# Kernel tuning notes

Hardware: AMD Instinct MI355X
Metric: run time of the kernel (lower is better)

Reference implementation:

```python
import jax, jax.numpy as jnp
import numpy as np

B, T, D = 256, 128, 64
H, A, O = 512, 128, 32


def setup_inputs() -> dict:
    key = jax.random.key(0)
    ks = jax.random.split(key, 16)
    u = lambda k, sh, lo, hi: jax.random.uniform(k, sh, jnp.float32, lo, hi)
    return {
        "x_states": jax.random.normal(ks[0], (B, T, D), jnp.float32),
        "x_dts": jax.random.uniform(ks[1], (B, T), jnp.float32) * 0.1,
        # StepwiseAttention params (stored [in, out])
        "Wq": u(ks[2], (D, A), -0.1, 0.1), "bq": u(ks[3], (A,), -0.1, 0.1),
        "Wk": u(ks[4], (H, A), -0.1, 0.1), "bk": u(ks[5], (A,), -0.1, 0.1),
        "Wv": u(ks[6], (H, A), -0.1, 0.1), "bv": u(ks[7], (A,), -0.1, 0.1),
        # LTCAttentionCell params
        "W_gd": u(ks[8], (D + H + A, 2 * H), -0.1, 0.1),
        "b_gd": u(ks[9], (2 * H,), -0.1, 0.1),
        "W_tau": u(ks[10], (H, H), -0.1, 0.1),
        "b_tau": u(ks[11], (H,), -0.1, 0.1),
        "gleak": u(ks[12], (H,), 0.001, 1.0),
        "cm": u(ks[13], (H,), 0.4, 0.6),
        # output head
        "W_fc": u(ks[14], (H, O), -0.1, 0.1),
        "b_fc": u(ks[15], (O,), -0.1, 0.1),
    }


def _forward(x_states, x_dts, Wq, bq, Wk, bk, Wv, bv,
             W_gd, b_gd, W_tau, b_tau, gleak, cm, W_fc, b_fc):
    scale = jnp.sqrt(jnp.asarray(A, jnp.float32))
    leak = jax.nn.softplus(cm) + jax.nn.softplus(gleak)  # [H]

    def dhdt(h, x_t, ctx):
        combined = jnp.concatenate([x_t, h, ctx], axis=1)        # [B, D+H+A]
        gd = combined @ W_gd + b_gd                              # [B, 2H]
        gate, dyn = jnp.split(gd, 2, axis=1)
        tau = jax.nn.softplus(h @ W_tau + b_tau)                 # [B, H]
        num = jax.nn.sigmoid(gate) * jnp.tanh(dyn) - h
        return num / (tau + leak + 1e-6)

    def step(carry, inp):
        h, hist = carry            # h [B,H], hist [B,T,H]
        t, x_t, dt = inp           # t scalar, x_t [B,D], dt [B]
        # stepwise attention over history h_1..h_t
        Q = x_t @ Wq + bq                                        # [B, A]
        K = hist @ Wk + bk                                       # [B, T, A]
        V = hist @ Wv + bv                                       # [B, T, A]
        scores = jnp.einsum('ba,bta->bt', Q, K) / scale          # [B, T]
        valid = jnp.arange(T) < t
        scores = jnp.where(valid[None, :], scores, -1e9)
        w = jax.nn.softmax(scores, axis=-1)
        ctx = jnp.einsum('bt,bta->ba', w, V)
        ctx = jnp.where(t > 0, ctx, jnp.zeros_like(ctx))         # empty history -> 0
        # one RK4 step (torchdiffeq 'rk4' = 3/8-rule variant), step size dt per sample
        dtc = dt[:, None]
        k1 = dhdt(h, x_t, ctx)
        k2 = dhdt(h + dtc * k1 / 3.0, x_t, ctx)
        k3 = dhdt(h + dtc * (k2 - k1 / 3.0), x_t, ctx)
        k4 = dhdt(h + dtc * (k1 - k2 + k3), x_t, ctx)
        h_next = h + dtc * (k1 + 3.0 * k2 + 3.0 * k3 + k4) / 8.0
        hist = jax.lax.dynamic_update_slice(hist, h_next[:, None, :], (0, t, 0))
        return (h_next, hist), None

    h0 = jnp.zeros((B, H), jnp.float32)
    hist0 = jnp.zeros((B, T, H), jnp.float32)
    xs = (jnp.arange(T), jnp.swapaxes(x_states, 0, 1), jnp.swapaxes(x_dts, 0, 1))
    (h_final, _), _ = jax.lax.scan(step, (h0, hist0), xs)
    return h_final @ W_fc + b_fc                                 # [B, O]


def reference(x_states, x_dts, Wq, bq, Wk, bk, Wv, bv,
              W_gd, b_gd, W_tau, b_tau, gleak, cm, W_fc, b_fc):
    return _forward(x_states, x_dts, Wq, bq, Wk, bk, Wv, bv,
                    W_gd, b_gd, W_tau, b_tau, gleak, cm, W_fc, b_fc)
```

## Files before the change

kernel.cpp:

```cpp
#include <hip/hip_runtime.h>
#include <math.h>

#define B_ 256
#define T_ 128
#define D_ 64
#define H_ 512
#define A_ 128
#define O_ 32

typedef __attribute__((ext_vector_type(8))) short short8;
typedef __attribute__((ext_vector_type(8))) unsigned short ushort8;
typedef __attribute__((ext_vector_type(4))) float floatx4;
typedef __attribute__((ext_vector_type(4))) unsigned int uintx4;
typedef unsigned long long ull;

__device__ __forceinline__ float sp_(float x) {
    return fmaxf(x, 0.f) + log1pf(expf(-fabsf(x)));
}
__device__ __forceinline__ float sigm_(float x) {
    return 1.f / (1.f + expf(-x));
}
__device__ __forceinline__ unsigned short f2bf_(float f) {
    unsigned int u = __float_as_uint(f);
    return (unsigned short)((u + 0x7FFFu + ((u >> 16) & 1u)) >> 16);
}
__device__ __forceinline__ float bf2f_(unsigned short u) {
    return __uint_as_float(((unsigned)u) << 16);
}

__device__ __forceinline__ void ld16sc(uintx4& d, const void* p) {
    asm volatile("global_load_dwordx4 %0, %1, off sc0 sc1"
                 : "=v"(d) : "v"(p) : "memory");
}
__device__ __forceinline__ void ld4sc(float& d, const void* p) {
    asm volatile("global_load_dword %0, %1, off sc0 sc1"
                 : "=v"(d) : "v"(p) : "memory");
}
__device__ __forceinline__ void vmwait4(uintx4& a, uintx4& b, uintx4& c,
                                        uintx4& d) {
    asm volatile("s_waitcnt vmcnt(0)"
                 : "+v"(a), "+v"(b), "+v"(c), "+v"(d)::"memory");
}
__device__ __forceinline__ void vmwait8(uintx4& a, uintx4& b, uintx4& c,
                                        uintx4& d, uintx4& e, uintx4& f,
                                        uintx4& g, uintx4& h) {
    asm volatile("s_waitcnt vmcnt(0)"
                 : "+v"(a), "+v"(b), "+v"(c), "+v"(d), "+v"(e), "+v"(f),
                   "+v"(g), "+v"(h)::"memory");
}
__device__ __forceinline__ void vmwait16f(float& a0, float& a1, float& a2,
                                          float& a3, float& a4, float& a5,
                                          float& a6, float& a7, float& b0,
                                          float& b1, float& b2, float& b3,
                                          float& b4, float& b5, float& b6,
                                          float& b7) {
    asm volatile("s_waitcnt vmcnt(0)"
                 : "+v"(a0), "+v"(a1), "+v"(a2), "+v"(a3), "+v"(a4), "+v"(a5),
                   "+v"(a6), "+v"(a7), "+v"(b0), "+v"(b1), "+v"(b2), "+v"(b3),
                   "+v"(b4), "+v"(b5), "+v"(b6), "+v"(b7)::"memory");
}
__device__ __forceinline__ floatx4 u2f_(uintx4 u) {
    union { uintx4 u; floatx4 f; } c;
    c.u = u;
    return c.f;
}

__device__ __forceinline__ void stf_(float* p, float v) {
    __hip_atomic_store(p, v, __ATOMIC_RELAXED, __HIP_MEMORY_SCOPE_SYSTEM);
}
__device__ __forceinline__ void st64_(ull* p, ull v) {
    __hip_atomic_store(p, v, __ATOMIC_RELAXED, __HIP_MEMORY_SCOPE_SYSTEM);
}

__global__ void init_kernel(unsigned short* __restrict__ hpack,
                            unsigned* __restrict__ bar) {
    int i = blockIdx.x * 256 + threadIdx.x;
    if (i < B_ * H_) hpack[i] = 0;
    if (i < 8192) bar[i] = 0u;
}

__global__ void pack_w_kernel(const float* __restrict__ W_gd,
                              const float* __restrict__ W_tau,
                              const float* __restrict__ Wk,
                              const float* __restrict__ Wv,
                              unsigned short* __restrict__ Wpack) {
    int gid = blockIdx.x * 256 + threadIdx.x;
    if (gid >= 1114112) return;
    int j = gid & 7;
    int l = (gid >> 3) & 63;
    int kpart = (l >> 4) * 8 + j;
    int npart = l & 15;
    float v;
    if (gid < 786432) {
        int f = gid >> 9;
        int s = f % 3;
        int rem = f / 3;
        int kb = rem & 15, ct = rem >> 4;
        int k = kb * 32 + kpart;
        int c = ct * 16 + npart;
        if (s == 0)      v = W_gd[(size_t)(D_ + k) * 1024 + c];
        else if (s == 1) v = W_gd[(size_t)(D_ + k) * 1024 + 512 + c];
        else             v = W_tau[(size_t)k * 512 + c];
    } else if (gid < 851968) {
        int r = gid - 786432;
        int f = r >> 9;
        int s = f & 1, kb = (f >> 1) & 1, ct = f >> 2;
        int k = kb * 32 + kpart;
        int c = ct * 16 + npart;
        v = W_gd[(size_t)k * 1024 + s * 512 + c];
    } else if (gid < 983040) {
        int r = gid - 851968;
        int f = r >> 9;
        int s = f & 1, kb = (f >> 1) & 3, ct = f >> 3;
        int k = kb * 32 + kpart;
        int c = ct * 16 + npart;
        v = W_gd[(size_t)(D_ + H_ + k) * 1024 + s * 512 + c];
    } else {
        int r = gid - 983040;
        int f = r >> 9;
        int kb = f & 15, c4 = f >> 4;
        int k = kb * 32 + kpart;
        int n = (c4 & 7) * 16 + npart;
        v = (c4 < 8) ? Wk[(size_t)k * A_ + n] : Wv[(size_t)k * A_ + n];
    }
    Wpack[gid] = f2bf_(v);
}

__device__ __forceinline__ void gsyncF(unsigned* flags, int j, unsigned cnt) {
    asm volatile("s_waitcnt vmcnt(0)" ::: "memory");
    __syncthreads();
    if (threadIdx.x == 0)
        __hip_atomic_store(flags + j * 64, cnt, __ATOMIC_RELAXED,
                           __HIP_MEMORY_SCOPE_SYSTEM);
    if (threadIdx.x < 8) {
        while (__hip_atomic_load(flags + threadIdx.x * 64, __ATOMIC_RELAXED,
                                 __HIP_MEMORY_SCOPE_SYSTEM) < cnt) {
            __builtin_amdgcn_s_sleep(1);
        }
    }
    __syncthreads();
}

struct P {
    const float *x, *dts, *Wq, *bq, *bk, *bv, *b_gd, *b_tau, *gleak, *cm,
        *W_fc, *b_fc;
    float *h, *ctx, *out, *Kpart, *Vpart;
    unsigned short* Kh;
    const unsigned short *Wy, *Wx, *Wc, *Wkv;
    unsigned short *hpack, *yapack, *ybpack;
    unsigned* bar;
};

__global__ __launch_bounds__(256, 1) void fused_kernel(P p) {
    const int tid = threadIdx.x;
    const int bid = blockIdx.x;
    const int lane = tid & 63;
    const int wave = tid >> 6;
    const int g = bid & 15;
    const int j = bid >> 4;
    const int ct = j * 4 + wave;
    unsigned* flags = p.bar + g * 512;
    unsigned cnt = 0;

    __shared__ float WqL[D_ * 129];
    __shared__ float xs4[2][D_];
    __shared__ float q4[2][A_];
    __shared__ float sc4[2][T_];
    __shared__ float red[2][2];
    __shared__ __align__(16) unsigned short AsL[32 * 256];
    __shared__ __align__(16) unsigned short ypbuf[4 * 256];
    __shared__ __align__(16) unsigned short As2[2 * 512];
    __shared__ unsigned short VhL[2][A_][136];

    const int quad = lane >> 4;
    const int c = ct * 16 + (lane & 15);
    const float btau = p.b_tau[c];
    const float lk = sp_(p.cm[c]) + sp_(p.gleak[c]) + 1e-6f;
    const float bgd_g = p.b_gd[c];
    const float bgd_d = p.b_gd[512 + c];
    const int aoff = (quad >> 1) * 256 + (lane & 15) * 16 + (quad & 1) * 8;
    const int ypw = wave * 256 + (lane & 15);

    const int sub = tid >> 7;
    const int tl = tid & 127;
    const int r = g * 16 + j * 2 + sub;
    const int rrow = r & 15;

    short8 wg[16], wd[16], wt[16];
    short8 wxg[2], wxd[2], wcg[4], wcd[4];
    {
        const short8* Wy8 = (const short8*)p.Wy;
        #pragma unroll
        for (int kb = 0; kb < 16; ++kb) {
            wg[kb] = Wy8[((ct * 16 + kb) * 3 + 0) * 64 + lane];
            wd[kb] = Wy8[((ct * 16 + kb) * 3 + 1) * 64 + lane];
            wt[kb] = Wy8[((ct * 16 + kb) * 3 + 2) * 64 + lane];
        }
        const short8* Wx8 = (const short8*)p.Wx;
        const short8* Wc8 = (const short8*)p.Wc;
        #pragma unroll
        for (int kb = 0; kb < 2; ++kb) {
            wxg[kb] = Wx8[((ct * 2 + kb) * 2 + 0) * 64 + lane];
            wxd[kb] = Wx8[((ct * 2 + kb) * 2 + 1) * 64 + lane];
        }
        #pragma unroll
        for (int kb = 0; kb < 4; ++kb) {
            wcg[kb] = Wc8[((ct * 4 + kb) * 2 + 0) * 64 + lane];
            wcd[kb] = Wc8[((ct * 4 + kb) * 2 + 1) * 64 + lane];
        }
    }

    for (int i = tid; i < D_ * A_; i += 256) {
        int d = i >> 7, a = i & 127;
        WqL[d * 129 + a] = p.Wq[i];
    }

    floatx4 hreg = {0.f, 0.f, 0.f, 0.f};
    floatx4 rk1, rk2, rk3, baseg, based, ycur, dt4;

    const short8* Wkv8 = (const short8*)p.Wkv;

    __syncthreads();

    for (int t = 0; t < T_; ++t) {
        {
            if (t > 0) {
                float kk[8], vv[8];
                #pragma unroll
                for (int jj = 0; jj < 8; ++jj) {
                    ld4sc(kk[jj],
                          p.Kpart + ((g * 8 + jj) * 16 + rrow) * 128 + tl);
                    ld4sc(vv[jj],
                          p.Vpart + ((g * 8 + jj) * 16 + rrow) * 128 + tl);
                }
                vmwait16f(kk[0], kk[1], kk[2], kk[3], kk[4], kk[5], kk[6],
                          kk[7], vv[0], vv[1], vv[2], vv[3], vv[4], vv[5],
                          vv[6], vv[7]);
                float ks = p.bk[tl], vs = p.bv[tl];
                #pragma unroll
                for (int jj = 0; jj < 8; ++jj) {
                    ks += kk[jj];
                    vs += vv[jj];
                }
                p.Kh[(size_t)(r * T_ + (t - 1)) * A_ + tl] = f2bf_(ks);
                VhL[sub][tl][t - 1] = f2bf_(vs);
            }
            if (tl < 16)
                ((float4*)xs4[sub])[tl] =
                    ((const float4*)&p.x[(r * T_ + t) * D_])[tl];
            __syncthreads();
            float qa = p.bq[tl];
            #pragma unroll 8
            for (int d = 0; d < D_; ++d) qa += xs4[sub][d] * WqL[d * 129 + tl];
            q4[sub][tl] = qa;
            __syncthreads();
            if (t == 0) {
                stf_(p.ctx + r * A_ + tl, 0.f);
            } else {
                const float rscale = 0.08838834764831845f;
                const int grp = tl >> 4, ln = tl & 15;
                float qv[8];
                #pragma unroll
                for (int i = 0; i < 8; ++i) qv[i] = q4[sub][ln * 8 + i];
                for (int s = grp; s < t; s += 8) {
                    ushort8 k8 = *((const ushort8*)(p.Kh +
                                     (size_t)(r * T_ + s) * A_) + ln);
                    float a2 = 0.f;
                    #pragma unroll
                    for (int i = 0; i < 8; ++i) a2 += bf2f_(k8[i]) * qv[i];
                    #pragma unroll
                    for (int off = 8; off > 0; off >>= 1)
                        a2 += __shfl_xor(a2, off, 16);
                    if (ln == 0) sc4[sub][s] = a2 * rscale;
                }
                __syncthreads();
                float mloc = -1e30f;
                for (int s = tl; s < t; s += 128) mloc = fmaxf(mloc, sc4[sub][s]);
                #pragma unroll
                for (int off = 32; off > 0; off >>= 1)
                    mloc = fmaxf(mloc, __shfl_xor(mloc, off, 64));
                if (lane == 0) red[sub][wave & 1] = mloc;
                __syncthreads();
                float m = fmaxf(red[sub][0], red[sub][1]);
                float ssum = 0.f;
                for (int s = tl; s < t; s += 128) {
                    float e = expf(sc4[sub][s] - m);
                    sc4[sub][s] = e;
                    ssum += e;
                }
                #pragma unroll
                for (int off = 32; off > 0; off >>= 1)
                    ssum += __shfl_xor(ssum, off, 64);
                __syncthreads();
                if (lane == 0) red[sub][wave & 1] = ssum;
                __syncthreads();
                float rs = 1.f / (red[sub][0] + red[sub][1]);
                const unsigned short* Vrow = &VhL[sub][tl][0];
                float ca0 = 0.f, ca1 = 0.f;
                int s0 = 0;
                for (; s0 + 16 <= t; s0 += 16) {
                    ushort8 v0 = *(const ushort8*)(Vrow + s0);
                    ushort8 v1 = *(const ushort8*)(Vrow + s0 + 8);
                    #pragma unroll
                    for (int i = 0; i < 8; ++i) {
                        ca0 += sc4[sub][s0 + i] * bf2f_(v0[i]);
                        ca1 += sc4[sub][s0 + 8 + i] * bf2f_(v1[i]);
                    }
                }
                if (s0 + 8 <= t) {
                    ushort8 v0 = *(const ushort8*)(Vrow + s0);
                    #pragma unroll
                    for (int i = 0; i < 8; ++i)
                        ca0 += sc4[sub][s0 + i] * bf2f_(v0[i]);
                    s0 += 8;
                }
                for (; s0 < t; ++s0) ca0 += sc4[sub][s0] * bf2f_(Vrow[s0]);
                stf_(p.ctx + r * A_ + tl, (ca0 + ca1) * rs);
            }
        }
        gsyncF(flags, j, ++cnt);

        {
            {
                const unsigned short* src = p.hpack + g * 8192;
                uintx4 av[4];
                #pragma unroll
                for (int i = 0; i < 4; ++i)
                    ld16sc(av[i], src + (size_t)tid * 8 + i * 2048);
                vmwait4(av[0], av[1], av[2], av[3]);
                #pragma unroll
                for (int i = 0; i < 4; ++i)
                    ((uintx4*)AsL)[tid + i * 256] = av[i];
            }
            const int mrow = lane & 15;
            const int kq = lane >> 4;
            const float* crow = &p.ctx[(g * 16 + mrow) * A_];
            uintx4 cc[8];
            #pragma unroll
            for (int kb = 0; kb < 4; ++kb) {
                ld16sc(cc[2 * kb], crow + kb * 32 + kq * 8);
                ld16sc(cc[2 * kb + 1], crow + kb * 32 + kq * 8 + 4);
            }
            vmwait8(cc[0], cc[1], cc[2], cc[3], cc[4], cc[5], cc[6], cc[7]);
            __syncthreads();

            #pragma unroll
            for (int i = 0; i < 4; ++i)
                dt4[i] = p.dts[(g * 16 + quad * 4 + i) * T_ + t];

            floatx4 bg = {0.f, 0.f, 0.f, 0.f};
            floatx4 bd = {0.f, 0.f, 0.f, 0.f};
            const float4* xrow =
                (const float4*)&p.x[((g * 16 + mrow) * T_ + t) * D_];
            #pragma unroll
            for (int kb = 0; kb < 2; ++kb) {
                float4 u = xrow[kb * 8 + kq * 2], v = xrow[kb * 8 + kq * 2 + 1];
                short8 ax;
                ax[0] = (short)f2bf_(u.x); ax[1] = (short)f2bf_(u.y);
                ax[2] = (short)f2bf_(u.z); ax[3] = (short)f2bf_(u.w);
                ax[4] = (short)f2bf_(v.x); ax[5] = (short)f2bf_(v.y);
                ax[6] = (short)f2bf_(v.z); ax[7] = (short)f2bf_(v.w);
                bg = __builtin_amdgcn_mfma_f32_16x16x32_bf16(ax, wxg[kb], bg, 0, 0, 0);
                bd = __builtin_amdgcn_mfma_f32_16x16x32_bf16(ax, wxd[kb], bd, 0, 0, 0);
            }
            #pragma unroll
            for (int kb = 0; kb < 4; ++kb) {
                floatx4 f0 = u2f_(cc[2 * kb]), f1 = u2f_(cc[2 * kb + 1]);
                short8 ac;
                ac[0] = (short)f2bf_(f0[0]); ac[1] = (short)f2bf_(f0[1]);
                ac[2] = (short)f2bf_(f0[2]); ac[3] = (short)f2bf_(f0[3]);
                ac[4] = (short)f2bf_(f1[0]); ac[5] = (short)f2bf_(f1[1]);
                ac[6] = (short)f2bf_(f1[2]); ac[7] = (short)f2bf_(f1[3]);
                bg = __builtin_amdgcn_mfma_f32_16x16x32_bf16(ac, wcg[kb], bg, 0, 0, 0);
                bd = __builtin_amdgcn_mfma_f32_16x16x32_bf16(ac, wcd[kb], bd, 0, 0, 0);
            }
            floatx4 ag = {0.f, 0.f, 0.f, 0.f};
            floatx4 ad = {0.f, 0.f, 0.f, 0.f};
            floatx4 at = {0.f, 0.f, 0.f, 0.f};
            #pragma unroll
            for (int kb = 0; kb < 16; ++kb) {
                short8 a = *(const short8*)(AsL + kb * 512 + aoff);
                ag = __builtin_amdgcn_mfma_f32_16x16x32_bf16(a, wg[kb], ag, 0, 0, 0);
                ad = __builtin_amdgcn_mfma_f32_16x16x32_bf16(a, wd[kb], ad, 0, 0, 0);
                at = __builtin_amdgcn_mfma_f32_16x16x32_bf16(a, wt[kb], at, 0, 0, 0);
            }
            #pragma unroll
            for (int i = 0; i < 4; ++i) {
                baseg[i] = bg[i] + bgd_g;
                based[i] = bd[i] + bgd_d;
                float gate = ag[i] + baseg[i];
                float dyn = ad[i] + based[i];
                float tau = sp_(at[i] + btau);
                float ki = (sigm_(gate) * tanhf(dyn) - hreg[i]) / (tau + lk);
                rk1[i] = ki;
                float yn = hreg[i] + dt4[i] * ki * (1.f / 3.f);
                ycur[i] = yn;
                ypbuf[ypw + (quad * 4 + i) * 16] = f2bf_(yn);
            }
            __syncthreads();
            st64_((ull*)p.yapack + g * 2048 + j * 256 + tid,
                  ((const ull*)ypbuf)[tid]);
        }
        gsyncF(flags, j, ++cnt);

        #pragma unroll 1
        for (int stage = 2; stage <= 4; ++stage) {
            const unsigned short* ysrc =
                (stage == 2) ? p.yapack : (stage == 3) ? p.ybpack : p.yapack;
            unsigned short* ydst =
                (stage == 2) ? p.ybpack : (stage == 3) ? p.yapack : p.hpack;
            {
                const unsigned short* src = ysrc + g * 8192;
                uintx4 av[4];
                #pragma unroll
                for (int i = 0; i < 4; ++i)
                    ld16sc(av[i], src + (size_t)tid * 8 + i * 2048);
                vmwait4(av[0], av[1], av[2], av[3]);
                #pragma unroll
                for (int i = 0; i < 4; ++i)
                    ((uintx4*)AsL)[tid + i * 256] = av[i];
            }
            __syncthreads();
            floatx4 ag = {0.f, 0.f, 0.f, 0.f};
            floatx4 ad = {0.f, 0.f, 0.f, 0.f};
            floatx4 at = {0.f, 0.f, 0.f, 0.f};
            #pragma unroll
            for (int kb = 0; kb < 16; ++kb) {
                short8 a = *(const short8*)(AsL + kb * 512 + aoff);
                ag = __builtin_amdgcn_mfma_f32_16x16x32_bf16(a, wg[kb], ag, 0, 0, 0);
                ad = __builtin_amdgcn_mfma_f32_16x16x32_bf16(a, wd[kb], ad, 0, 0, 0);
                at = __builtin_amdgcn_mfma_f32_16x16x32_bf16(a, wt[kb], at, 0, 0, 0);
            }
            const int lane_p = ((c >> 3) & 3) * 16;
            #pragma unroll
            for (int i = 0; i < 4; ++i) {
                float gate = ag[i] + baseg[i];
                float dyn = ad[i] + based[i];
                float tau = sp_(at[i] + btau);
                float ki = (sigm_(gate) * tanhf(dyn) - ycur[i]) / (tau + lk);
                float yn;
                if (stage == 2) {
                    rk2[i] = ki;
                    yn = hreg[i] + dt4[i] * (ki - rk1[i] * (1.f / 3.f));
                } else if (stage == 3) {
                    rk3[i] = ki;
                    yn = hreg[i] + dt4[i] * (rk1[i] - rk2[i] + ki);
                } else {
                    yn = hreg[i] +
                         dt4[i] * (rk1[i] + 3.f * rk2[i] + 3.f * rk3[i] + ki) * 0.125f;
                    hreg[i] = yn;
                }
                ycur[i] = yn;
                ypbuf[ypw + (quad * 4 + i) * 16] = f2bf_(yn);
                if (stage == 4)
                    As2[(wave >> 1) * 512 + (c & 7) +
                        (lane_p + quad * 4 + i) * 8] = f2bf_(yn);
            }
            __syncthreads();
            st64_((ull*)ydst + g * 2048 + j * 256 + tid,
                  ((const ull*)ypbuf)[tid]);
            if (stage == 4) {
                #pragma unroll
                for (int h4 = 0; h4 < 4; ++h4) {
                    const int c4 = wave + h4 * 4;
                    floatx4 acc = {0.f, 0.f, 0.f, 0.f};
                    #pragma unroll
                    for (int kk2 = 0; kk2 < 2; ++kk2) {
                        short8 a = *(const short8*)(As2 + (kk2 * 64 + lane) * 8);
                        acc = __builtin_amdgcn_mfma_f32_16x16x32_bf16(
                            a, Wkv8[(c4 * 16 + (j * 2 + kk2)) * 64 + lane], acc,
                            0, 0, 0);
                    }
                    const int ac = (c4 & 7) * 16 + (lane & 15);
                    float* part = (c4 < 8) ? p.Kpart : p.Vpart;
                    #pragma unroll
                    for (int i = 0; i < 4; ++i)
                        stf_(part + ((g * 8 + j) * 16 + quad * 4 + i) * 128 + ac,
                             acc[i]);
                }
            }
            gsyncF(flags, j, ++cnt);
        }
    }

    #pragma unroll
    for (int i = 0; i < 4; ++i)
        stf_(p.h + (g * 16 + quad * 4 + i) * H_ + c, hreg[i]);
    gsyncF(flags, j, ++cnt);
    {
        const int o = tl & 31, ks = tl >> 5;
        float acc = 0.f;
        const float* hrow = p.h + r * H_ + ks * 128;
        const float* wcol = p.W_fc + ks * 128 * O_ + o;
        #pragma unroll 1
        for (int rd = 0; rd < 4; ++rd) {
            uintx4 hh[8];
            #pragma unroll
            for (int i = 0; i < 8; ++i)
                ld16sc(hh[i], hrow + rd * 32 + i * 4);
            vmwait8(hh[0], hh[1], hh[2], hh[3], hh[4], hh[5], hh[6], hh[7]);
            #pragma unroll
            for (int i = 0; i < 8; ++i) {
                floatx4 f = u2f_(hh[i]);
                #pragma unroll
                for (int e = 0; e < 4; ++e)
                    acc += f[e] * wcol[(rd * 32 + i * 4 + e) * O_];
            }
        }
        sc4[sub][tl] = acc;
        __syncthreads();
        if (ks == 0)
            p.out[r * O_ + o] = acc + sc4[sub][o + 32] + sc4[sub][o + 64] +
                                sc4[sub][o + 96] + p.b_fc[o];
    }
}

extern "C" void kernel_launch(void* const* d_in, const int* in_sizes, int n_in,
                              void* d_out, int out_size, void* d_ws,
                              size_t ws_size, hipStream_t stream) {
    (void)in_sizes; (void)n_in; (void)out_size; (void)ws_size;
    P p;
    p.x = (const float*)d_in[0];
    p.dts = (const float*)d_in[1];
    p.Wq = (const float*)d_in[2];
    p.bq = (const float*)d_in[3];
    const float* Wk = (const float*)d_in[4];
    p.bk = (const float*)d_in[5];
    const float* Wv = (const float*)d_in[6];
    p.bv = (const float*)d_in[7];
    const float* W_gd = (const float*)d_in[8];
    p.b_gd = (const float*)d_in[9];
    const float* W_tau = (const float*)d_in[10];
    p.b_tau = (const float*)d_in[11];
    p.gleak = (const float*)d_in[12];
    p.cm = (const float*)d_in[13];
    p.W_fc = (const float*)d_in[14];
    p.b_fc = (const float*)d_in[15];
    p.out = (float*)d_out;

    float* ws = (float*)d_ws;
    p.h = ws;
    p.ctx = p.h + B_ * H_;
    p.Kpart = p.ctx + B_ * A_;
    p.Vpart = p.Kpart + 262144;
    unsigned short* Wpack = (unsigned short*)(p.Vpart + 262144);
    p.Wy = Wpack;
    p.Wx = Wpack + 786432;
    p.Wc = Wpack + 851968;
    p.Wkv = Wpack + 983040;
    p.hpack = Wpack + 1114112;
    p.yapack = p.hpack + B_ * H_;
    p.ybpack = p.yapack + B_ * H_;
    p.Kh = p.ybpack + B_ * H_;
    p.bar = (unsigned*)(p.Kh + (size_t)B_ * T_ * A_);

    init_kernel<<<512, 256, 0, stream>>>(p.hpack, p.bar);
    pack_w_kernel<<<4352, 256, 0, stream>>>(W_gd, W_tau, Wk, Wv, Wpack);

    fused_kernel<<<dim3(128), dim3(256), 0, stream>>>(p);
}
```

Before: 3.597 ms.

## Replace group barriers with per-stage sentinel flags and fine-grained consumer polling

Swaps the full intra-group barrier after each RK stage for per-producer sentinel counters. Consumers poll only the sentinels of the producers whose data they need, issuing their data loads together with the sentinel check. A third ping-pong buffer (ycpack) is added so that stages can run ahead without overwriting data still being read. This is meant to shorten the 5 global barrier waits per timestep, at the cost of repeated speculative loads while spinning and more complex memory-ordering reasoning.

```diff
diff --git a/kernel.cpp b/kernel.cpp
--- a/kernel.cpp
+++ b/kernel.cpp
@@ -35,6 +35,18 @@
 __device__ __forceinline__ void ld4sc(float& d, const void* p) {
     asm volatile("global_load_dword %0, %1, off sc0 sc1"
                  : "=v"(d) : "v"(p) : "memory");
+}
+__device__ __forceinline__ void ld4su(unsigned& d, const void* p) {
+    asm volatile("global_load_dword %0, %1, off sc0 sc1"
+                 : "=v"(d) : "v"(p) : "memory");
+}
+__device__ __forceinline__ void st64sc(ull* p, ull v) {
+    asm volatile("global_store_dwordx2 %0, %1, off sc0 sc1"
+                 :: "v"(p), "v"(v) : "memory");
+}
+__device__ __forceinline__ void stu32sc(unsigned* p, unsigned v) {
+    asm volatile("global_store_dword %0, %1, off sc0 sc1"
+                 :: "v"(p), "v"(v) : "memory");
 }
 __device__ __forceinline__ void vmwait4(uintx4& a, uintx4& b, uintx4& c,
                                         uintx4& d) {
@@ -59,16 +71,27 @@
                    "+v"(a6), "+v"(a7), "+v"(b0), "+v"(b1), "+v"(b2), "+v"(b3),
                    "+v"(b4), "+v"(b5), "+v"(b6), "+v"(b7)::"memory");
 }
+__device__ __forceinline__ void vmwait8u(unsigned& a, unsigned& b, unsigned& c,
+                                         unsigned& d, unsigned& e, unsigned& f,
+                                         unsigned& g, unsigned& h) {
+    asm volatile("s_waitcnt vmcnt(0)"
+                 : "+v"(a), "+v"(b), "+v"(c), "+v"(d), "+v"(e), "+v"(f),
+                   "+v"(g), "+v"(h)::"memory");
+}
+__device__ __forceinline__ void vmwait4u(unsigned& a, unsigned& b, unsigned& c,
+                                         unsigned& d) {
+    asm volatile("s_waitcnt vmcnt(0)"
+                 : "+v"(a), "+v"(b), "+v"(c), "+v"(d)::"memory");
+}
+__device__ __forceinline__ void vmwait1u(unsigned& a) {
+    asm volatile("s_waitcnt vmcnt(0)" : "+v"(a)::"memory");
+}
 __device__ __forceinline__ floatx4 u2f_(uintx4 u) {
     union { uintx4 u; floatx4 f; } c;
     c.u = u;
     return c.f;
 }
-
 __device__ __forceinline__ void stf_(float* p, float v) {
-    __hip_atomic_store(p, v, __ATOMIC_RELAXED, __HIP_MEMORY_SCOPE_SYSTEM);
-}
-__device__ __forceinline__ void st64_(ull* p, ull v) {
     __hip_atomic_store(p, v, __ATOMIC_RELAXED, __HIP_MEMORY_SCOPE_SYSTEM);
 }
 
@@ -76,7 +99,7 @@
                             unsigned* __restrict__ bar) {
     int i = blockIdx.x * 256 + threadIdx.x;
     if (i < B_ * H_) hpack[i] = 0;
-    if (i < 8192) bar[i] = 0u;
+    if (i < 18432) bar[i] = 0u;
 }
 
 __global__ void pack_w_kernel(const float* __restrict__ W_gd,
@@ -129,14 +152,15 @@
 __device__ __forceinline__ void gsyncF(unsigned* flags, int j, unsigned cnt) {
     asm volatile("s_waitcnt vmcnt(0)" ::: "memory");
     __syncthreads();
-    if (threadIdx.x == 0)
-        __hip_atomic_store(flags + j * 64, cnt, __ATOMIC_RELAXED,
-                           __HIP_MEMORY_SCOPE_SYSTEM);
+    if (threadIdx.x == 0) stu32sc(flags + j * 64, cnt);
     if (threadIdx.x < 8) {
-        while (__hip_atomic_load(flags + threadIdx.x * 64, __ATOMIC_RELAXED,
-                                 __HIP_MEMORY_SCOPE_SYSTEM) < cnt) {
+        unsigned v;
+        do {
+            ld4su(v, flags + threadIdx.x * 64);
+            vmwait1u(v);
+            if (v >= cnt) break;
             __builtin_amdgcn_s_sleep(1);
-        }
+        } while (true);
     }
     __syncthreads();
 }
@@ -147,7 +171,7 @@
     float *h, *ctx, *out, *Kpart, *Vpart;
     unsigned short* Kh;
     const unsigned short *Wy, *Wx, *Wc, *Wkv;
-    unsigned short *hpack, *yapack, *ybpack;
+    unsigned short *hpack, *yapack, *ybpack, *ycpack;
     unsigned* bar;
 };
 
@@ -160,7 +184,8 @@
     const int j = bid >> 4;
     const int ct = j * 4 + wave;
     unsigned* flags = p.bar + g * 512;
-    unsigned cnt = 0;
+    unsigned* senbase = p.bar + 8192;
+    #define SEN(kind, src) (senbase + (((kind)*16 + g) * 8 + (src)) * 16)
 
     __shared__ float WqL[D_ * 129];
     __shared__ float xs4[2][D_];
@@ -224,18 +249,42 @@
 
     for (int t = 0; t < T_; ++t) {
         {
+            float kk[8], vv[8];
+            uintx4 av[4];
+            {
+                const unsigned short* src = p.hpack + g * 8192;
+                const unsigned expv = (unsigned)t;
+                unsigned s0, s1, s2, s3, s4, s5, s6, s7;
+                for (;;) {
+                    #pragma unroll
+                    for (int jj = 0; jj < 8; ++jj) {
+                        ld4sc(kk[jj],
+                              p.Kpart + ((g * 8 + jj) * 16 + rrow) * 128 + tl);
+                        ld4sc(vv[jj],
+                              p.Vpart + ((g * 8 + jj) * 16 + rrow) * 128 + tl);
+                    }
+                    #pragma unroll
+                    for (int i = 0; i < 4; ++i)
+                        ld16sc(av[i], src + (size_t)tid * 8 + i * 2048);
+                    ld4su(s0, SEN(4, 0)); ld4su(s1, SEN(4, 1));
+                    ld4su(s2, SEN(4, 2)); ld4su(s3, SEN(4, 3));
+                    ld4su(s4, SEN(4, 4)); ld4su(s5, SEN(4, 5));
+                    ld4su(s6, SEN(4, 6)); ld4su(s7, SEN(4, 7));
+                    vmwait16f(kk[0], kk[1], kk[2], kk[3], kk[4], kk[5], kk[6],
+                              kk[7], vv[0], vv[1], vv[2], vv[3], vv[4], vv[5],
+                              vv[6], vv[7]);
+                    vmwait4(av[0], av[1], av[2], av[3]);
+                    vmwait8u(s0, s1, s2, s3, s4, s5, s6, s7);
+                    if (s0 >= expv && s1 >= expv && s2 >= expv && s3 >= expv &&
+                        s4 >= expv && s5 >= expv && s6 >= expv && s7 >= expv)
+                        break;
+                    __builtin_amdgcn_s_sleep(1);
+                }
+            }
+            #pragma unroll
+            for (int i = 0; i < 4; ++i)
+                ((uintx4*)AsL)[tid + i * 256] = av[i];
             if (t > 0) {
-                float kk[8], vv[8];
-                #pragma unroll
-                for (int jj = 0; jj < 8; ++jj) {
-                    ld4sc(kk[jj],
-                          p.Kpart + ((g * 8 + jj) * 16 + rrow) * 128 + tl);
-                    ld4sc(vv[jj],
-                          p.Vpart + ((g * 8 + jj) * 16 + rrow) * 128 + tl);
-                }
-                vmwait16f(kk[0], kk[1], kk[2], kk[3], kk[4], kk[5], kk[6],
-                          kk[7], vv[0], vv[1], vv[2], vv[3], vv[4], vv[5],
-                          vv[6], vv[7]);
                 float ks = p.bk[tl], vs = p.bv[tl];
                 #pragma unroll
                 for (int jj = 0; jj < 8; ++jj) {
@@ -318,32 +367,32 @@
                 stf_(p.ctx + r * A_ + tl, (ca0 + ca1) * rs);
             }
         }
-        gsyncF(flags, j, ++cnt);
+        asm volatile("s_waitcnt vmcnt(0)" ::: "memory");
+        __syncthreads();
+        if (tid == 0) stu32sc(SEN(0, j), (unsigned)(t + 1));
 
         {
-            {
-                const unsigned short* src = p.hpack + g * 8192;
-                uintx4 av[4];
-                #pragma unroll
-                for (int i = 0; i < 4; ++i)
-                    ld16sc(av[i], src + (size_t)tid * 8 + i * 2048);
-                vmwait4(av[0], av[1], av[2], av[3]);
-                #pragma unroll
-                for (int i = 0; i < 4; ++i)
-                    ((uintx4*)AsL)[tid + i * 256] = av[i];
-            }
             const int mrow = lane & 15;
-            const int kq = lane >> 4;
             const float* crow = &p.ctx[(g * 16 + mrow) * A_];
             uintx4 cc[8];
-            #pragma unroll
-            for (int kb = 0; kb < 4; ++kb) {
-                ld16sc(cc[2 * kb], crow + kb * 32 + kq * 8);
-                ld16sc(cc[2 * kb + 1], crow + kb * 32 + kq * 8 + 4);
-            }
-            vmwait8(cc[0], cc[1], cc[2], cc[3], cc[4], cc[5], cc[6], cc[7]);
-            __syncthreads();
-
+            {
+                const unsigned* senp = SEN(0, mrow >> 1);
+                const unsigned expv = (unsigned)(t + 1);
+                unsigned sv;
+                for (;;) {
+                    #pragma unroll
+                    for (int kb = 0; kb < 4; ++kb) {
+                        ld16sc(cc[2 * kb], crow + kb * 32 + quad * 8);
+                        ld16sc(cc[2 * kb + 1], crow + kb * 32 + quad * 8 + 4);
+                    }
+                    ld4su(sv, senp);
+                    vmwait8(cc[0], cc[1], cc[2], cc[3], cc[4], cc[5], cc[6],
+                            cc[7]);
+                    vmwait1u(sv);
+                    if (sv >= expv) break;
+                    __builtin_amdgcn_s_sleep(1);
+                }
+            }
             #pragma unroll
             for (int i = 0; i < 4; ++i)
                 dt4[i] = p.dts[(g * 16 + quad * 4 + i) * T_ + t];
@@ -354,7 +403,7 @@
                 (const float4*)&p.x[((g * 16 + mrow) * T_ + t) * D_];
             #pragma unroll
             for (int kb = 0; kb < 2; ++kb) {
-                float4 u = xrow[kb * 8 + kq * 2], v = xrow[kb * 8 + kq * 2 + 1];
+                float4 u = xrow[kb * 8 + quad * 2], v = xrow[kb * 8 + quad * 2 + 1];
                 short8 ax;
                 ax[0] = (short)f2bf_(u.x); ax[1] = (short)f2bf_(u.y);
                 ax[2] = (short)f2bf_(u.z); ax[3] = (short)f2bf_(u.w);
@@ -398,24 +447,40 @@
                 ypbuf[ypw + (quad * 4 + i) * 16] = f2bf_(yn);
             }
             __syncthreads();
-            st64_((ull*)p.yapack + g * 2048 + j * 256 + tid,
-                  ((const ull*)ypbuf)[tid]);
+            st64sc((ull*)p.yapack + g * 2048 + j * 256 + tid,
+                   ((const ull*)ypbuf)[tid]);
         }
-        gsyncF(flags, j, ++cnt);
+        asm volatile("s_waitcnt vmcnt(0)" ::: "memory");
+        __syncthreads();
+        if (tid == 0) stu32sc(SEN(1, j), (unsigned)(t + 1));
 
         #pragma unroll 1
         for (int stage = 2; stage <= 4; ++stage) {
             const unsigned short* ysrc =
-                (stage == 2) ? p.yapack : (stage == 3) ? p.ybpack : p.yapack;
+                (stage == 2) ? p.yapack : (stage == 3) ? p.ybpack : p.ycpack;
             unsigned short* ydst =
-                (stage == 2) ? p.ybpack : (stage == 3) ? p.yapack : p.hpack;
+                (stage == 2) ? p.ybpack : (stage == 3) ? p.ycpack : p.hpack;
+            const int senk = stage - 1;
             {
                 const unsigned short* src = ysrc + g * 8192;
+                const unsigned expv = (unsigned)(t + 1);
+                const int sb = tid >> 7;
                 uintx4 av[4];
-                #pragma unroll
-                for (int i = 0; i < 4; ++i)
-                    ld16sc(av[i], src + (size_t)tid * 8 + i * 2048);
-                vmwait4(av[0], av[1], av[2], av[3]);
+                unsigned s0, s1, s2, s3;
+                for (;;) {
+                    #pragma unroll
+                    for (int i = 0; i < 4; ++i)
+                        ld16sc(av[i], src + (size_t)tid * 8 + i * 2048);
+                    ld4su(s0, SEN(senk, sb + 0));
+                    ld4su(s1, SEN(senk, sb + 2));
+                    ld4su(s2, SEN(senk, sb + 4));
+                    ld4su(s3, SEN(senk, sb + 6));
+                    vmwait4(av[0], av[1], av[2], av[3]);
+                    vmwait4u(s0, s1, s2, s3);
+                    if (s0 >= expv && s1 >= expv && s2 >= expv && s3 >= expv)
+                        break;
+                    __builtin_amdgcn_s_sleep(1);
+                }
                 #pragma unroll
                 for (int i = 0; i < 4; ++i)
                     ((uintx4*)AsL)[tid + i * 256] = av[i];
@@ -457,8 +522,8 @@
                         (lane_p + quad * 4 + i) * 8] = f2bf_(yn);
             }
             __syncthreads();
-            st64_((ull*)ydst + g * 2048 + j * 256 + tid,
-                  ((const ull*)ypbuf)[tid]);
+            st64sc((ull*)ydst + g * 2048 + j * 256 + tid,
+                   ((const ull*)ypbuf)[tid]);
             if (stage == 4) {
                 #pragma unroll
                 for (int h4 = 0; h4 < 4; ++h4) {
@@ -479,14 +544,16 @@
                              acc[i]);
                 }
             }
-            gsyncF(flags, j, ++cnt);
+            asm volatile("s_waitcnt vmcnt(0)" ::: "memory");
+            __syncthreads();
+            if (tid == 0) stu32sc(SEN(stage, j), (unsigned)(t + 1));
         }
     }
 
     #pragma unroll
     for (int i = 0; i < 4; ++i)
         stf_(p.h + (g * 16 + quad * 4 + i) * H_ + c, hreg[i]);
-    gsyncF(flags, j, ++cnt);
+    gsyncF(flags, j, 1u);
     {
         const int o = tl & 31, ks = tl >> 5;
         float acc = 0.f;
@@ -513,6 +580,7 @@
             p.out[r * O_ + o] = acc + sc4[sub][o + 32] + sc4[sub][o + 64] +
                                 sc4[sub][o + 96] + p.b_fc[o];
     }
+    #undef SEN
 }
 
 extern "C" void kernel_launch(void* const* d_in, const int* in_sizes, int n_in,
@@ -551,7 +619,8 @@
     p.hpack = Wpack + 1114112;
     p.yapack = p.hpack + B_ * H_;
     p.ybpack = p.yapack + B_ * H_;
-    p.Kh = p.ybpack + B_ * H_;
+    p.ycpack = p.ybpack + B_ * H_;
+    p.Kh = p.ycpack + B_ * H_;
     p.bar = (unsigned*)(p.Kh + (size_t)B_ * T_ * A_);
 
     init_kernel<<<512, 256, 0, stream>>>(p.hpack, p.bar);
```

Measured after the change: 3.529 ms. Within noise of the previous version (-1.9%).
